# Kernel optimization log

Measured on AMD Instinct MI355X. Metric: run time of the kernel, lower is better.

## Reference

```python
import jax, jax.numpy as jnp
import numpy as np

N_EXPERTS = 8
D_MODEL = 512
HIDDEN = 1408
TOTAL_TOKENS = 32768  # 4096 tokens per expert, equal contiguous segments


def setup_inputs() -> dict:
    key = jax.random.key(0)
    k1, k2, k3 = jax.random.split(key, 3)
    sorted_x = jax.random.normal(k1, (TOTAL_TOKENS, D_MODEL), dtype=jnp.float32)
    # weights init: normal(std=0.02) as in the torch module
    w12 = 0.02 * jax.random.normal(k2, (N_EXPERTS, 2 * HIDDEN, D_MODEL), dtype=jnp.float32)
    w3 = 0.02 * jax.random.normal(k3, (N_EXPERTS, D_MODEL, HIDDEN), dtype=jnp.float32)
    tpe = TOTAL_TOKENS // N_EXPERTS
    expert_starts = jnp.arange(N_EXPERTS, dtype=jnp.int32) * tpe
    expert_ends = expert_starts + tpe
    return {"sorted_x": sorted_x, "w12": w12, "w3": w3,
            "expert_starts": expert_starts, "expert_ends": expert_ends}


def reference(sorted_x, w12, w3, expert_starts, expert_ends):
    """Grouped SwiGLU expert MLP over tokens pre-sorted by expert.

    setup_inputs() produces equal-sized contiguous expert segments, so each
    expert processes tpe = T // E tokens (fixed-size grouped GEMM).
    """
    E, twoH, D = w12.shape
    T = sorted_x.shape[0]
    tpe = T // E  # tokens per expert segment

    # gather each expert's contiguous token block: (E, tpe, D)
    x_e = jax.vmap(lambda s: jax.lax.dynamic_slice(sorted_x, (s, 0), (tpe, D)))(expert_starts)

    # grouped GEMM 1 (fused gate+up): (E, tpe, 2H)
    h12 = jnp.einsum('etd,ehd->eth', x_e, w12).astype(jnp.float32)
    h1, h2 = jnp.split(h12, 2, axis=-1)
    h = jax.nn.silu(h1) * h2  # SwiGLU

    # grouped GEMM 2 (down-proj): (E, tpe, D)
    out = jnp.einsum('eth,edh->etd', h.astype(sorted_x.dtype), w3).astype(jnp.float32)
    # segments are contiguous and in expert order -> concat == reshape
    return out.reshape(T, D)
```

## Files before the change

### kernel.cpp

```cpp
#include <hip/hip_runtime.h>
#include <stdint.h>

#define TPE 4096
#define DM 512
#define HID 1408
#define NE 8

typedef unsigned short u16;
typedef __attribute__((ext_vector_type(8))) __bf16 bf16x8;
typedef __attribute__((ext_vector_type(4))) float f32x4;

__device__ __forceinline__ u16 f2bf(float f) {
  union { float f; uint32_t u; } v; v.f = f;
  uint32_t u = v.u;
  u += 0x7fffu + ((u >> 16) & 1u);
  return (u16)(u >> 16);
}

__global__ void cvt_f32_bf16(const float* __restrict__ in, u16* __restrict__ out, int n4) {
  int i = blockIdx.x * blockDim.x + threadIdx.x;
  if (i >= n4) return;
  float4 v = reinterpret_cast<const float4*>(in)[i];
  union { u16 s[4]; uint2 u2; } o;
  o.s[0] = f2bf(v.x); o.s[1] = f2bf(v.y); o.s[2] = f2bf(v.z); o.s[3] = f2bf(v.w);
  reinterpret_cast<uint2*>(out)[i] = o.u2;
}

__device__ __forceinline__ void stage_tile64(u16* lds, const u16* g, int lda,
                                             int wave, int lane) {
  const int srow = lane >> 3;
  const int gchunk = (lane & 7) ^ srow;
#pragma unroll
  for (int r = 0; r < 4; ++r) {
    const int row0 = (wave * 4 + r) * 8;
    const u16* gp = g + (size_t)(row0 + srow) * lda + gchunk * 8;
    u16* lp = lds + row0 * 64;
    __builtin_amdgcn_global_load_lds((const __attribute__((address_space(1))) void*)gp,
                                     (__attribute__((address_space(3))) void*)lp,
                                     16, 0, 0);
  }
}

__device__ __forceinline__ bf16x8 read_frag(const u16* lds, int row, int kchunk) {
  return *reinterpret_cast<const bf16x8*>(&lds[row * 64 + (((kchunk ^ (row & 7)) << 3))]);
}

__global__ __launch_bounds__(256, 2)
void gemm1_swiglu(const u16* __restrict__ xb, const u16* __restrict__ w12b,
                  u16* __restrict__ hb) {
  __shared__ u16 sA[128 * 64];
  __shared__ u16 sBg[128 * 64];
  __shared__ u16 sBu[128 * 64];
  const int mt = blockIdx.x, nt = blockIdx.y, e = blockIdx.z;
  const int tid = threadIdx.x, wave = tid >> 6, lane = tid & 63;
  const int wm = wave >> 1, wn = wave & 1;
  const int quad = lane >> 4, rr = lane & 15;

  const u16* A  = xb + (size_t)(e * TPE + mt * 128) * DM;
  const u16* Bg = w12b + (size_t)e * (2 * HID) * DM + (size_t)(nt * 128) * DM;
  const u16* Bu = Bg + (size_t)HID * DM;

  f32x4 zero = {0.f, 0.f, 0.f, 0.f};
  f32x4 accg[4][4], accu[4][4];
#pragma unroll
  for (int i = 0; i < 4; ++i)
#pragma unroll
    for (int j = 0; j < 4; ++j) { accg[i][j] = zero; accu[i][j] = zero; }

  for (int k0 = 0; k0 < DM; k0 += 64) {
    stage_tile64(sA, A + k0, DM, wave, lane);
    stage_tile64(sBg, Bg + k0, DM, wave, lane);
    stage_tile64(sBu, Bu + k0, DM, wave, lane);
    __syncthreads();

#pragma unroll
    for (int kk = 0; kk < 2; ++kk) {
      const int kc = kk * 4 + quad;
      bf16x8 af[4], bg[4], bu[4];
#pragma unroll
      for (int mi = 0; mi < 4; ++mi)
        af[mi] = read_frag(sA, wm * 64 + mi * 16 + rr, kc);
#pragma unroll
      for (int ni = 0; ni < 4; ++ni) {
        bg[ni] = read_frag(sBg, wn * 64 + ni * 16 + rr, kc);
        bu[ni] = read_frag(sBu, wn * 64 + ni * 16 + rr, kc);
      }
#pragma unroll
      for (int mi = 0; mi < 4; ++mi)
#pragma unroll
        for (int ni = 0; ni < 4; ++ni) {
          accg[mi][ni] = __builtin_amdgcn_mfma_f32_16x16x32_bf16(af[mi], bg[ni], accg[mi][ni], 0, 0, 0);
          accu[mi][ni] = __builtin_amdgcn_mfma_f32_16x16x32_bf16(af[mi], bu[ni], accu[mi][ni], 0, 0, 0);
        }
    }
    __syncthreads();
  }

  const size_t rowbase = (size_t)(e * TPE + mt * 128 + wm * 64);
  const int colbase = nt * 128 + wn * 64;
#pragma unroll
  for (int mi = 0; mi < 4; ++mi)
#pragma unroll
    for (int ni = 0; ni < 4; ++ni)
#pragma unroll
      for (int r2 = 0; r2 < 4; ++r2) {
        float g = accg[mi][ni][r2];
        float u = accu[mi][ni][r2];
        float s = (g / (1.f + __expf(-g))) * u;
        size_t row = rowbase + mi * 16 + quad * 4 + r2;
        int col = colbase + ni * 16 + rr;
        hb[row * HID + col] = f2bf(s);
      }
}

__global__ __launch_bounds__(256, 2)
void gemm2(const u16* __restrict__ hb, const u16* __restrict__ w3b,
           float* __restrict__ out) {
  __shared__ u16 sA[128 * 64];
  __shared__ u16 sB[128 * 64];
  const int mt = blockIdx.x, nt = blockIdx.y, e = blockIdx.z;
  const int tid = threadIdx.x, wave = tid >> 6, lane = tid & 63;
  const int wm = wave >> 1, wn = wave & 1;
  const int quad = lane >> 4, rr = lane & 15;

  const u16* A = hb + (size_t)(e * TPE + mt * 128) * HID;
  const u16* B = w3b + (size_t)e * DM * HID + (size_t)(nt * 128) * HID;

  f32x4 zero = {0.f, 0.f, 0.f, 0.f};
  f32x4 acc[4][4];
#pragma unroll
  for (int i = 0; i < 4; ++i)
#pragma unroll
    for (int j = 0; j < 4; ++j) acc[i][j] = zero;

  for (int k0 = 0; k0 < HID; k0 += 64) {
    stage_tile64(sA, A + k0, HID, wave, lane);
    stage_tile64(sB, B + k0, HID, wave, lane);
    __syncthreads();

#pragma unroll
    for (int kk = 0; kk < 2; ++kk) {
      const int kc = kk * 4 + quad;
      bf16x8 af[4], bfr[4];
#pragma unroll
      for (int mi = 0; mi < 4; ++mi)
        af[mi] = read_frag(sA, wm * 64 + mi * 16 + rr, kc);
#pragma unroll
      for (int ni = 0; ni < 4; ++ni)
        bfr[ni] = read_frag(sB, wn * 64 + ni * 16 + rr, kc);
#pragma unroll
      for (int mi = 0; mi < 4; ++mi)
#pragma unroll
        for (int ni = 0; ni < 4; ++ni)
          acc[mi][ni] = __builtin_amdgcn_mfma_f32_16x16x32_bf16(af[mi], bfr[ni], acc[mi][ni], 0, 0, 0);
    }
    __syncthreads();
  }

  const size_t rowbase = (size_t)(e * TPE + mt * 128 + wm * 64);
  const int colbase = nt * 128 + wn * 64;
#pragma unroll
  for (int mi = 0; mi < 4; ++mi)
#pragma unroll
    for (int ni = 0; ni < 4; ++ni)
#pragma unroll
      for (int r2 = 0; r2 < 4; ++r2) {
        size_t row = rowbase + mi * 16 + quad * 4 + r2;
        int col = colbase + ni * 16 + rr;
        out[row * DM + col] = acc[mi][ni][r2];
      }
}

extern "C" void kernel_launch(void* const* d_in, const int* in_sizes, int n_in,
                              void* d_out, int out_size, void* d_ws, size_t ws_size,
                              hipStream_t stream) {
  (void)in_sizes; (void)n_in; (void)out_size; (void)ws_size;
  const float* x   = (const float*)d_in[0];
  const float* w12 = (const float*)d_in[1];
  const float* w3  = (const float*)d_in[2];
  float* out = (float*)d_out;

  char* ws = (char*)d_ws;
  u16* xb   = (u16*)(ws);
  u16* w12b = (u16*)(ws + (size_t)33554432);
  u16* w3b  = (u16*)(ws + (size_t)33554432 + 23068672);
  u16* hb   = (u16*)(ws + (size_t)33554432 + 23068672 + 11534336);

  const int n4x   = (32768 * 512) / 4;
  const int n4w12 = (NE * 2816 * 512) / 4;
  const int n4w3  = (NE * 512 * 1408) / 4;
  cvt_f32_bf16<<<n4x / 256, 256, 0, stream>>>(x, xb, n4x);
  cvt_f32_bf16<<<n4w12 / 256, 256, 0, stream>>>(w12, w12b, n4w12);
  cvt_f32_bf16<<<n4w3 / 256, 256, 0, stream>>>(w3, w3b, n4w3);

  gemm1_swiglu<<<dim3(32, 11, NE), 256, 0, stream>>>(xb, w12b, hb);
  gemm2<<<dim3(32, 4, NE), 256, 0, stream>>>(hb, w3b, out);
}
```

Before: 336.4 us.

## Widen gemm2 N-tile to 256 and fuse the three conversion kernels

The down-projection GEMM now uses a 128x256 output tile per block, so each wave computes 64x128 with twice as many accumulators. This halves how often the A (hidden activation) tiles are re-read and halves the grid to 512 blocks. The three fp32-to-bf16 conversion launches are merged into one kernel that picks its source by index, which saves launch overhead. The price is higher register and LDS pressure in gemm2, which may reduce occupancy below the two blocks per CU declared in launch bounds.

```diff
diff --git a/kernel.cpp b/kernel.cpp
--- a/kernel.cpp
+++ b/kernel.cpp
@@ -5,6 +5,10 @@
 #define DM 512
 #define HID 1408
 #define NE 8
+
+#define N4X   4194304
+#define N4W12 2883584
+#define N4W3  1441792
 
 typedef unsigned short u16;
 typedef __attribute__((ext_vector_type(8))) __bf16 bf16x8;
@@ -17,22 +21,28 @@
   return (u16)(u >> 16);
 }
 
-__global__ void cvt_f32_bf16(const float* __restrict__ in, u16* __restrict__ out, int n4) {
+__global__ void cvt_all(const float* __restrict__ x, const float* __restrict__ w12,
+                        const float* __restrict__ w3, u16* __restrict__ xb,
+                        u16* __restrict__ w12b, u16* __restrict__ w3b) {
   int i = blockIdx.x * blockDim.x + threadIdx.x;
-  if (i >= n4) return;
-  float4 v = reinterpret_cast<const float4*>(in)[i];
+  const float* src; u16* dst; int off;
+  if (i < N4X)               { src = x;   dst = xb;   off = i; }
+  else if (i < N4X + N4W12)  { src = w12; dst = w12b; off = i - N4X; }
+  else                       { src = w3;  dst = w3b;  off = i - N4X - N4W12; }
+  float4 v = reinterpret_cast<const float4*>(src)[off];
   union { u16 s[4]; uint2 u2; } o;
   o.s[0] = f2bf(v.x); o.s[1] = f2bf(v.y); o.s[2] = f2bf(v.z); o.s[3] = f2bf(v.w);
-  reinterpret_cast<uint2*>(out)[i] = o.u2;
-}
-
+  reinterpret_cast<uint2*>(dst)[off] = o.u2;
+}
+
+template <int ROWS>
 __device__ __forceinline__ void stage_tile64(u16* lds, const u16* g, int lda,
                                              int wave, int lane) {
   const int srow = lane >> 3;
   const int gchunk = (lane & 7) ^ srow;
 #pragma unroll
-  for (int r = 0; r < 4; ++r) {
-    const int row0 = (wave * 4 + r) * 8;
+  for (int r = 0; r < ROWS / 32; ++r) {
+    const int row0 = (wave * (ROWS / 32) + r) * 8;
     const u16* gp = g + (size_t)(row0 + srow) * lda + gchunk * 8;
     u16* lp = lds + row0 * 64;
     __builtin_amdgcn_global_load_lds((const __attribute__((address_space(1))) void*)gp,
@@ -68,9 +78,9 @@
     for (int j = 0; j < 4; ++j) { accg[i][j] = zero; accu[i][j] = zero; }
 
   for (int k0 = 0; k0 < DM; k0 += 64) {
-    stage_tile64(sA, A + k0, DM, wave, lane);
-    stage_tile64(sBg, Bg + k0, DM, wave, lane);
-    stage_tile64(sBu, Bu + k0, DM, wave, lane);
+    stage_tile64<128>(sA, A + k0, DM, wave, lane);
+    stage_tile64<128>(sBg, Bg + k0, DM, wave, lane);
+    stage_tile64<128>(sBu, Bu + k0, DM, wave, lane);
     __syncthreads();
 
 #pragma unroll
@@ -117,52 +127,52 @@
 void gemm2(const u16* __restrict__ hb, const u16* __restrict__ w3b,
            float* __restrict__ out) {
   __shared__ u16 sA[128 * 64];
-  __shared__ u16 sB[128 * 64];
+  __shared__ u16 sB[256 * 64];
   const int mt = blockIdx.x, nt = blockIdx.y, e = blockIdx.z;
   const int tid = threadIdx.x, wave = tid >> 6, lane = tid & 63;
   const int wm = wave >> 1, wn = wave & 1;
   const int quad = lane >> 4, rr = lane & 15;
 
   const u16* A = hb + (size_t)(e * TPE + mt * 128) * HID;
-  const u16* B = w3b + (size_t)e * DM * HID + (size_t)(nt * 128) * HID;
+  const u16* B = w3b + (size_t)e * DM * HID + (size_t)(nt * 256) * HID;
 
   f32x4 zero = {0.f, 0.f, 0.f, 0.f};
-  f32x4 acc[4][4];
+  f32x4 acc[4][8];
 #pragma unroll
   for (int i = 0; i < 4; ++i)
 #pragma unroll
-    for (int j = 0; j < 4; ++j) acc[i][j] = zero;
+    for (int j = 0; j < 8; ++j) acc[i][j] = zero;
 
   for (int k0 = 0; k0 < HID; k0 += 64) {
-    stage_tile64(sA, A + k0, HID, wave, lane);
-    stage_tile64(sB, B + k0, HID, wave, lane);
+    stage_tile64<128>(sA, A + k0, HID, wave, lane);
+    stage_tile64<256>(sB, B + k0, HID, wave, lane);
     __syncthreads();
 
 #pragma unroll
     for (int kk = 0; kk < 2; ++kk) {
       const int kc = kk * 4 + quad;
-      bf16x8 af[4], bfr[4];
+      bf16x8 af[4], bfr[8];
 #pragma unroll
       for (int mi = 0; mi < 4; ++mi)
         af[mi] = read_frag(sA, wm * 64 + mi * 16 + rr, kc);
 #pragma unroll
-      for (int ni = 0; ni < 4; ++ni)
-        bfr[ni] = read_frag(sB, wn * 64 + ni * 16 + rr, kc);
-#pragma unroll
-      for (int mi = 0; mi < 4; ++mi)
-#pragma unroll
-        for (int ni = 0; ni < 4; ++ni)
+      for (int ni = 0; ni < 8; ++ni)
+        bfr[ni] = read_frag(sB, wn * 128 + ni * 16 + rr, kc);
+#pragma unroll
+      for (int mi = 0; mi < 4; ++mi)
+#pragma unroll
+        for (int ni = 0; ni < 8; ++ni)
           acc[mi][ni] = __builtin_amdgcn_mfma_f32_16x16x32_bf16(af[mi], bfr[ni], acc[mi][ni], 0, 0, 0);
     }
     __syncthreads();
   }
 
   const size_t rowbase = (size_t)(e * TPE + mt * 128 + wm * 64);
-  const int colbase = nt * 128 + wn * 64;
+  const int colbase = nt * 256 + wn * 128;
 #pragma unroll
   for (int mi = 0; mi < 4; ++mi)
 #pragma unroll
-    for (int ni = 0; ni < 4; ++ni)
+    for (int ni = 0; ni < 8; ++ni)
 #pragma unroll
       for (int r2 = 0; r2 < 4; ++r2) {
         size_t row = rowbase + mi * 16 + quad * 4 + r2;
@@ -186,13 +196,9 @@
   u16* w3b  = (u16*)(ws + (size_t)33554432 + 23068672);
   u16* hb   = (u16*)(ws + (size_t)33554432 + 23068672 + 11534336);
 
-  const int n4x   = (32768 * 512) / 4;
-  const int n4w12 = (NE * 2816 * 512) / 4;
-  const int n4w3  = (NE * 512 * 1408) / 4;
-  cvt_f32_bf16<<<n4x / 256, 256, 0, stream>>>(x, xb, n4x);
-  cvt_f32_bf16<<<n4w12 / 256, 256, 0, stream>>>(w12, w12b, n4w12);
-  cvt_f32_bf16<<<n4w3 / 256, 256, 0, stream>>>(w3, w3b, n4w3);
+  const int n4 = N4X + N4W12 + N4W3;
+  cvt_all<<<n4 / 256, 256, 0, stream>>>(x, w12, w3, xb, w12b, w3b);
 
   gemm1_swiglu<<<dim3(32, 11, NE), 256, 0, stream>>>(xb, w12b, hb);
-  gemm2<<<dim3(32, 4, NE), 256, 0, stream>>>(hb, w3b, out);
-}
+  gemm2<<<dim3(32, 2, NE), 256, 0, stream>>>(hb, w3b, out);
+}
```

Result: faster. 313.9 us (-6.7%).
